# Optimization experiments

Hardware: AMD Instinct MI355X
Metric: run time of the kernel (lower is better)

Reference implementation:

```python
import jax, jax.numpy as jnp
import numpy as np

N = 131072
K = 27
FIN = 3
FOUT = 32
EPS = 1e-5


def _bn(h, gamma, beta, mean, var):
    return (h - mean) * jax.lax.rsqrt(var + EPS) * gamma + beta


def setup_inputs() -> dict:
    key = jax.random.key(0)
    ks = jax.random.split(key, 8)
    return {
        "x_feats": jax.random.normal(ks[0], (N, FIN), jnp.float32),
        "z_feats": jax.random.normal(ks[1], (N, FIN), jnp.float32),
        "nbr_idx": jax.random.randint(ks[2], (N, K), 0, N, jnp.int32),
        "w1": jax.random.normal(ks[3], (K, FIN, FOUT), jnp.float32) * 0.2,
        "bn1_gamma": jnp.ones((FOUT,), jnp.float32),
        "bn1_beta": jnp.zeros((FOUT,), jnp.float32),
        "bn1_mean": jax.random.normal(ks[4], (FOUT,), jnp.float32) * 0.1,
        "bn1_var": jax.random.uniform(ks[5], (FOUT,), jnp.float32, 0.5, 1.5),
        "w2": jax.random.normal(ks[6], (K, FOUT, FOUT), jnp.float32) * 0.1,
        "mlp_w": jax.random.normal(ks[7], (FIN, FOUT), jnp.float32) * 0.3,
        "mlp_b": jnp.zeros((FOUT,), jnp.float32),
        "mlp_gamma": jnp.ones((FOUT,), jnp.float32),
        "mlp_beta": jnp.zeros((FOUT,), jnp.float32),
        "mlp_mean": jnp.zeros((FOUT,), jnp.float32),
        "mlp_var": jnp.ones((FOUT,), jnp.float32),
    }


def reference(x_feats, z_feats, nbr_idx, w1, bn1_gamma, bn1_beta, bn1_mean,
              bn1_var, w2, mlp_w, mlp_b, mlp_gamma, mlp_beta, mlp_mean,
              mlp_var):
    # --- voxel branch: sparse conv (gather-GEMM) -> BN -> SiLU -> sparse conv
    g1 = x_feats[nbr_idx]                       # [N, K, FIN] irregular gather
    h = jnp.einsum('nkf,kfo->no', g1, w1)       # [N, FOUT]
    h = jax.nn.silu(_bn(h, bn1_gamma, bn1_beta, bn1_mean, bn1_var))
    g2 = h[nbr_idx]                             # [N, K, FOUT] irregular gather
    x_out = jnp.einsum('nkf,kfo->no', g2, w2)   # [N, FOUT]

    # --- point branch: SharedMLP = Linear -> BN -> ReLU
    z = z_feats @ mlp_w + mlp_b
    z = jax.nn.relu(_bn(z, mlp_gamma, mlp_beta, mlp_mean, mlp_var))

    # --- mixed_mix: fuse voxel and point features additively
    fused = x_out + z
    return (fused, fused)
```

## Files before the change

### kernel.cpp

```cpp
#include <hip/hip_runtime.h>
#include <math.h>

#define NN 131072
#define KK 27
#define KP 28
#define FIN 3
#define FOUT 32
#define EPS 1e-5f

typedef _Float16 f16;
typedef __attribute__((ext_vector_type(8))) _Float16 f16x8;
typedef __attribute__((ext_vector_type(16))) float f32x16;

__global__ __launch_bounds__(256) void pack_kernel(
    const float* __restrict__ w2, const float* __restrict__ w1,
    f16* __restrict__ w2p, float* __restrict__ w1p)
{
    const int t = blockIdx.x * 256 + threadIdx.x;
    if (t < KP * 1024) {
        const int k    = t >> 10;
        const int rem  = t & 1023;
        const int half = rem >> 9;
        const int l    = (rem >> 3) & 63;
        const int j    = rem & 7;
        const int krow = half * 16 + ((l >> 5) << 3) + j;
        const int n    = l & 31;
        w2p[t] = (k < KK) ? (f16)w2[k * (FOUT * FOUT) + krow * FOUT + n]
                          : (f16)0.f;
    } else {
        const int u = t - KP * 1024;
        if (u < KP * FIN * FOUT) {
            const int k = u / (FIN * FOUT);
            w1p[u] = (k < KK) ? w1[u] : 0.f;
        }
    }
}

__global__ __launch_bounds__(256) void pad_x_kernel(
    const float* __restrict__ x, float4* __restrict__ xp)
{
    const int n = blockIdx.x * 256 + threadIdx.x;
    if (n >= NN) return;
    const float* r = x + (size_t)n * 3;
    xp[n] = make_float4(r[0], r[1], r[2], 0.f);
}

__global__ __launch_bounds__(256) void conv1_kernel(
    const float4* __restrict__ xpad,
    const int*    __restrict__ nbr_idx,
    const float*  __restrict__ w1p,
    const float* __restrict__ g1,  const float* __restrict__ b1,
    const float* __restrict__ m1,  const float* __restrict__ v1,
    f16* __restrict__ h_out)
{
    __shared__ float racc[FOUT][128];

    const int tid   = threadIdx.x;
    const int khalf = tid >> 7;
    const int ln    = tid & 127;
    const int n     = blockIdx.x * 128 + ln;
    const int kb    = khalf * 14;

    int idxs[14];
    const int* nb = nbr_idx + (size_t)n * KK + kb;
#pragma unroll
    for (int i = 0; i < 14; ++i) {
        const int off = (kb + i < KK) ? i : 0;
        idxs[i] = nb[off];
    }
#pragma unroll
    for (int i = 0; i < 14; ++i) asm volatile("" : "+v"(idxs[i]));

    float acc[FOUT];
#pragma unroll
    for (int o = 0; o < FOUT; ++o) acc[o] = 0.f;

#pragma unroll
    for (int c = 0; c < 2; ++c) {
        float4 xs[7];
#pragma unroll
        for (int q = 0; q < 7; ++q)
            xs[q] = xpad[idxs[c * 7 + q]];
#pragma unroll
        for (int q = 0; q < 7; ++q) {
            const float* w = w1p + (kb + c * 7 + q) * (FIN * FOUT);
#pragma unroll
            for (int o = 0; o < FOUT; ++o) {
                float a = acc[o];
                a = fmaf(xs[q].x, w[o],            a);
                a = fmaf(xs[q].y, w[FOUT + o],     a);
                a = fmaf(xs[q].z, w[2 * FOUT + o], a);
                acc[o] = a;
            }
        }
    }

    if (khalf) {
#pragma unroll
        for (int o = 0; o < FOUT; ++o) racc[o][ln] = acc[o];
    }
    __syncthreads();
    if (khalf) return;

#pragma unroll
    for (int o = 0; o < FOUT; ++o) acc[o] += racc[o][ln];

    f16* hr = h_out + (size_t)n * FOUT;
#pragma unroll
    for (int g = 0; g < 4; ++g) {
        f16x8 hv;
#pragma unroll
        for (int j = 0; j < 8; ++j) {
            const int o = g * 8 + j;
            const float sc = g1[o] * rsqrtf(v1[o] + EPS);
            float v = (acc[o] - m1[o]) * sc + b1[o];
            v = v / (1.f + __expf(-v));
            hv[j] = (f16)v;
        }
        *(f16x8*)(hr + g * 8) = hv;
    }
}

__global__ __launch_bounds__(256) void conv2_mfma_kernel(
    const f16*   __restrict__ h,
    const int*   __restrict__ nbr_idx,
    const f16*   __restrict__ w2p,
    const float* __restrict__ z_feats,
    const float* __restrict__ mlp_w,
    const float* __restrict__ mlp_b,
    const float* __restrict__ mg, const float* __restrict__ mbe,
    const float* __restrict__ mm, const float* __restrict__ mv,
    float* __restrict__ out)
{
    const int lane = threadIdx.x & 63;
    const int wave = threadIdx.x >> 6;
    const int base = (blockIdx.x * 4 + wave) * 32;
    const int row  = lane & 31;
    const int hi   = lane >> 5;

    int idxs[KK];
    const int* nb = nbr_idx + (size_t)(base + row) * KK;
#pragma unroll
    for (int k = 0; k < KK; ++k) idxs[k] = nb[k];
#pragma unroll
    for (int k = 0; k < KK; ++k) asm volatile("" : "+v"(idxs[k]));

    f32x16 acc0 = {};
    f32x16 acc1 = {};

    const f16x8* bp = (const f16x8*)w2p;

    constexpr int D = 6;
    f16x8 A1[KK], A2[KK];

#pragma unroll
    for (int k = 0; k < D; ++k) {
        const f16* hr = h + (size_t)idxs[k] * FOUT + hi * 8;
        A1[k] = *(const f16x8*)hr;
        A2[k] = *(const f16x8*)(hr + 16);
    }

#pragma unroll
    for (int k = 0; k < KK; ++k) {
        if (k + D < KK) {
            const f16* hr = h + (size_t)idxs[k + D] * FOUT + hi * 8;
            A1[k + D] = *(const f16x8*)hr;
            A2[k + D] = *(const f16x8*)(hr + 16);
        }
        const f16x8 b1 = bp[k * 128 + lane];
        const f16x8 b2 = bp[k * 128 + 64 + lane];
        __builtin_amdgcn_s_setprio(1);
        acc0 = __builtin_amdgcn_mfma_f32_32x32x16_f16(A1[k], b1, acc0, 0, 0, 0);
        acc1 = __builtin_amdgcn_mfma_f32_32x32x16_f16(A2[k], b2, acc1, 0, 0, 0);
        __builtin_amdgcn_s_setprio(0);
    }

    const int n0 = lane & 31;
    const float wc0 = mlp_w[n0];
    const float wc1 = mlp_w[FOUT + n0];
    const float wc2 = mlp_w[2 * FOUT + n0];
    const float sc  = mg[n0] * rsqrtf(mv[n0] + EPS);
    const float bi  = mlp_b[n0];
    const float mmv = mm[n0];
    const float mbv = mbe[n0];

#pragma unroll
    for (int r = 0; r < 16; ++r) {
        const int m    = (r & 3) + ((r >> 2) << 3) + (hi << 2);
        const int node = base + m;
        const float* zr = z_feats + (size_t)node * FIN;
        float z = bi;
        z = fmaf(zr[0], wc0, z);
        z = fmaf(zr[1], wc1, z);
        z = fmaf(zr[2], wc2, z);
        z = (z - mmv) * sc + mbv;
        z = fmaxf(z, 0.f);
        const float v = acc0[r] + acc1[r] + z;
        out[(size_t)node * FOUT + n0] = v;
        out[(size_t)NN * FOUT + (size_t)node * FOUT + n0] = v;
    }
}

extern "C" void kernel_launch(void* const* d_in, const int* in_sizes, int n_in,
                              void* d_out, int out_size, void* d_ws, size_t ws_size,
                              hipStream_t stream) {
    const float* x_feats = (const float*)d_in[0];
    const float* z_feats = (const float*)d_in[1];
    const int*   nbr_idx = (const int*)d_in[2];
    const float* w1      = (const float*)d_in[3];
    const float* bn1_g   = (const float*)d_in[4];
    const float* bn1_b   = (const float*)d_in[5];
    const float* bn1_m   = (const float*)d_in[6];
    const float* bn1_v   = (const float*)d_in[7];
    const float* w2      = (const float*)d_in[8];
    const float* mlp_w   = (const float*)d_in[9];
    const float* mlp_b   = (const float*)d_in[10];
    const float* mlp_g   = (const float*)d_in[11];
    const float* mlp_be  = (const float*)d_in[12];
    const float* mlp_m   = (const float*)d_in[13];
    const float* mlp_v   = (const float*)d_in[14];

    const size_t OFF_W2P  = (size_t)8 * 1024 * 1024;
    const size_t OFF_W1P  = OFF_W2P + 64 * 1024;
    const size_t OFF_XPAD = (size_t)9 * 1024 * 1024;

    f16*    h    = (f16*)d_ws;
    f16*    w2p  = (f16*)((char*)d_ws + OFF_W2P);
    float*  w1p  = (float*)((char*)d_ws + OFF_W1P);
    float4* xpad = (float4*)((char*)d_ws + OFF_XPAD);
    float* out = (float*)d_out;

    const int pack_elems = KP * 1024 + KP * FIN * FOUT;
    pack_kernel<<<(pack_elems + 255) / 256, 256, 0, stream>>>(w2, w1, w2p, w1p);
    pad_x_kernel<<<NN / 256, 256, 0, stream>>>(x_feats, xpad);
    conv1_kernel<<<NN / 128, 256, 0, stream>>>(xpad, nbr_idx, w1p,
                                               bn1_g, bn1_b, bn1_m, bn1_v, h);
    conv2_mfma_kernel<<<NN / 128, 256, 0, stream>>>(h, nbr_idx, w2p, z_feats,
                                                    mlp_w, mlp_b, mlp_g, mlp_be,
                                                    mlp_m, mlp_v, out);
}
```

Before: 201.9 us.

## Transpose neighbor indices, split h into two halves, and restructure conv kernels

Adds a prep kernel that transposes nbr_idx into a k-major layout, so index loads in both conv kernels become coalesced, and fuses the x padding into it. The h buffer is split into two 16-channel halves, so each conv2 gather reads one 32-byte row per neighbor. Conv2 now runs two sequential MFMA passes with a one-step prefetch instead of a deep register prefetch, and sets a launch-bounds occupancy hint. Conv1 splits K four ways per block of 64 nodes. The cost is an extra write and read of a transposed index array, roughly 14 MB, plus a fallback path used when the workspace is too small.

```diff
diff --git a/kernel.cpp b/kernel.cpp
--- a/kernel.cpp
+++ b/kernel.cpp
@@ -36,6 +36,34 @@
     }
 }
 
+__global__ __launch_bounds__(256) void prep_kernel(
+    const int* __restrict__ nbr_idx, const float* __restrict__ x,
+    int* __restrict__ nbrT, float4* __restrict__ xpad)
+{
+    __shared__ int   lidx[64][29];
+    __shared__ float lx[192];
+    const int t  = threadIdx.x;
+    const int n0 = blockIdx.x * 64;
+
+    const int* src = nbr_idx + (size_t)n0 * KK;
+#pragma unroll
+    for (int j = 0; j < 7; ++j) {
+        const int f = j * 256 + t;
+        if (f < 64 * KK) lidx[f / KK][f % KK] = src[f];
+    }
+    if (t < 192) lx[t] = x[(size_t)n0 * 3 + t];
+    __syncthreads();
+
+    const int g = t >> 6, ln = t & 63;
+#pragma unroll
+    for (int j = 0; j < 7; ++j) {
+        const int k = g * 7 + j;
+        nbrT[(size_t)k * NN + n0 + ln] = (k < KK) ? lidx[ln][k] : 0;
+    }
+    if (t < 64)
+        xpad[n0 + t] = make_float4(lx[t * 3], lx[t * 3 + 1], lx[t * 3 + 2], 0.f);
+}
+
 __global__ __launch_bounds__(256) void pad_x_kernel(
     const float* __restrict__ x, float4* __restrict__ xp)
 {
@@ -45,67 +73,64 @@
     xp[n] = make_float4(r[0], r[1], r[2], 0.f);
 }
 
+template<bool TR>
 __global__ __launch_bounds__(256) void conv1_kernel(
     const float4* __restrict__ xpad,
+    const int*    __restrict__ nbrT,
     const int*    __restrict__ nbr_idx,
     const float*  __restrict__ w1p,
     const float* __restrict__ g1,  const float* __restrict__ b1,
     const float* __restrict__ m1,  const float* __restrict__ v1,
-    f16* __restrict__ h_out)
-{
-    __shared__ float racc[FOUT][128];
-
-    const int tid   = threadIdx.x;
-    const int khalf = tid >> 7;
-    const int ln    = tid & 127;
-    const int n     = blockIdx.x * 128 + ln;
-    const int kb    = khalf * 14;
-
-    int idxs[14];
-    const int* nb = nbr_idx + (size_t)n * KK + kb;
-#pragma unroll
-    for (int i = 0; i < 14; ++i) {
-        const int off = (kb + i < KK) ? i : 0;
-        idxs[i] = nb[off];
-    }
-#pragma unroll
-    for (int i = 0; i < 14; ++i) asm volatile("" : "+v"(idxs[i]));
+    f16* __restrict__ h0, f16* __restrict__ h1)
+{
+    __shared__ float racc[3][FOUT][64];
+    const int t  = threadIdx.x;
+    const int kg = t >> 6;
+    const int ln = t & 63;
+    const int n  = blockIdx.x * 64 + ln;
+
+    int idxs[7];
+#pragma unroll
+    for (int i = 0; i < 7; ++i) {
+        const int k = kg * 7 + i;
+        if (TR) idxs[i] = nbrT[(size_t)k * NN + n];
+        else    idxs[i] = (k < KK) ? nbr_idx[(size_t)n * KK + k] : 0;
+    }
+#pragma unroll
+    for (int i = 0; i < 7; ++i) asm volatile("" : "+v"(idxs[i]));
+
+    float4 xs[7];
+#pragma unroll
+    for (int i = 0; i < 7; ++i) xs[i] = xpad[idxs[i]];
 
     float acc[FOUT];
 #pragma unroll
     for (int o = 0; o < FOUT; ++o) acc[o] = 0.f;
 
 #pragma unroll
-    for (int c = 0; c < 2; ++c) {
-        float4 xs[7];
-#pragma unroll
-        for (int q = 0; q < 7; ++q)
-            xs[q] = xpad[idxs[c * 7 + q]];
-#pragma unroll
-        for (int q = 0; q < 7; ++q) {
-            const float* w = w1p + (kb + c * 7 + q) * (FIN * FOUT);
-#pragma unroll
-            for (int o = 0; o < FOUT; ++o) {
-                float a = acc[o];
-                a = fmaf(xs[q].x, w[o],            a);
-                a = fmaf(xs[q].y, w[FOUT + o],     a);
-                a = fmaf(xs[q].z, w[2 * FOUT + o], a);
-                acc[o] = a;
-            }
-        }
-    }
-
-    if (khalf) {
-#pragma unroll
-        for (int o = 0; o < FOUT; ++o) racc[o][ln] = acc[o];
+    for (int i = 0; i < 7; ++i) {
+        const float* w = w1p + (kg * 7 + i) * (FIN * FOUT);
+#pragma unroll
+        for (int o = 0; o < FOUT; ++o) {
+            float a = acc[o];
+            a = fmaf(xs[i].x, w[o],            a);
+            a = fmaf(xs[i].y, w[FOUT + o],     a);
+            a = fmaf(xs[i].z, w[2 * FOUT + o], a);
+            acc[o] = a;
+        }
+    }
+
+    if (kg) {
+#pragma unroll
+        for (int o = 0; o < FOUT; ++o) racc[kg - 1][o][ln] = acc[o];
     }
     __syncthreads();
-    if (khalf) return;
-
-#pragma unroll
-    for (int o = 0; o < FOUT; ++o) acc[o] += racc[o][ln];
-
-    f16* hr = h_out + (size_t)n * FOUT;
+    if (kg) return;
+
+#pragma unroll
+    for (int o = 0; o < FOUT; ++o)
+        acc[o] += racc[0][o][ln] + racc[1][o][ln] + racc[2][o][ln];
+
 #pragma unroll
     for (int g = 0; g < 4; ++g) {
         f16x8 hv;
@@ -117,12 +142,17 @@
             v = v / (1.f + __expf(-v));
             hv[j] = (f16)v;
         }
-        *(f16x8*)(hr + g * 8) = hv;
-    }
-}
-
-__global__ __launch_bounds__(256) void conv2_mfma_kernel(
-    const f16*   __restrict__ h,
+        f16* dst = (g < 2) ? (h0 + (size_t)n * 16 + (g & 1) * 8)
+                           : (h1 + (size_t)n * 16 + (g & 1) * 8);
+        *(f16x8*)dst = hv;
+    }
+}
+
+template<bool TR>
+__global__ __launch_bounds__(256, 4) void conv2_mfma_kernel(
+    const f16*   __restrict__ h0,
+    const f16*   __restrict__ h1,
+    const int*   __restrict__ nbrT,
     const int*   __restrict__ nbr_idx,
     const f16*   __restrict__ w2p,
     const float* __restrict__ z_feats,
@@ -139,40 +169,52 @@
     const int hi   = lane >> 5;
 
     int idxs[KK];
-    const int* nb = nbr_idx + (size_t)(base + row) * KK;
-#pragma unroll
-    for (int k = 0; k < KK; ++k) idxs[k] = nb[k];
+#pragma unroll
+    for (int k = 0; k < KK; ++k) {
+        if (TR) idxs[k] = nbrT[(size_t)k * NN + base + row];
+        else    idxs[k] = nbr_idx[(size_t)(base + row) * KK + k];
+    }
 #pragma unroll
     for (int k = 0; k < KK; ++k) asm volatile("" : "+v"(idxs[k]));
 
-    f32x16 acc0 = {};
-    f32x16 acc1 = {};
+    f32x16 accA = {};
+    f32x16 accB = {};
 
     const f16x8* bp = (const f16x8*)w2p;
 
-    constexpr int D = 6;
-    f16x8 A1[KK], A2[KK];
-
-#pragma unroll
-    for (int k = 0; k < D; ++k) {
-        const f16* hr = h + (size_t)idxs[k] * FOUT + hi * 8;
-        A1[k] = *(const f16x8*)hr;
-        A2[k] = *(const f16x8*)(hr + 16);
-    }
-
-#pragma unroll
-    for (int k = 0; k < KK; ++k) {
-        if (k + D < KK) {
-            const f16* hr = h + (size_t)idxs[k + D] * FOUT + hi * 8;
-            A1[k + D] = *(const f16x8*)hr;
-            A2[k + D] = *(const f16x8*)(hr + 16);
-        }
-        const f16x8 b1 = bp[k * 128 + lane];
-        const f16x8 b2 = bp[k * 128 + 64 + lane];
-        __builtin_amdgcn_s_setprio(1);
-        acc0 = __builtin_amdgcn_mfma_f32_32x32x16_f16(A1[k], b1, acc0, 0, 0, 0);
-        acc1 = __builtin_amdgcn_mfma_f32_32x32x16_f16(A2[k], b2, acc1, 0, 0, 0);
-        __builtin_amdgcn_s_setprio(0);
+    {
+        f16x8 a = *(const f16x8*)(h0 + (size_t)idxs[0] * 16 + hi * 8);
+        f16x8 b = bp[lane];
+#pragma unroll
+        for (int k = 0; k < KK; ++k) {
+            f16x8 na, nb2;
+            const bool more = (k + 1 < KK);
+            if (more) {
+                na  = *(const f16x8*)(h0 + (size_t)idxs[k + 1] * 16 + hi * 8);
+                nb2 = bp[(k + 1) * 128 + lane];
+            }
+            __builtin_amdgcn_s_setprio(1);
+            accA = __builtin_amdgcn_mfma_f32_32x32x16_f16(a, b, accA, 0, 0, 0);
+            __builtin_amdgcn_s_setprio(0);
+            if (more) { a = na; b = nb2; }
+        }
+    }
+    {
+        f16x8 a = *(const f16x8*)(h1 + (size_t)idxs[0] * 16 + hi * 8);
+        f16x8 b = bp[64 + lane];
+#pragma unroll
+        for (int k = 0; k < KK; ++k) {
+            f16x8 na, nb2;
+            const bool more = (k + 1 < KK);
+            if (more) {
+                na  = *(const f16x8*)(h1 + (size_t)idxs[k + 1] * 16 + hi * 8);
+                nb2 = bp[(k + 1) * 128 + 64 + lane];
+            }
+            __builtin_amdgcn_s_setprio(1);
+            accB = __builtin_amdgcn_mfma_f32_32x32x16_f16(a, b, accB, 0, 0, 0);
+            __builtin_amdgcn_s_setprio(0);
+            if (more) { a = na; b = nb2; }
+        }
     }
 
     const int n0 = lane & 31;
@@ -195,7 +237,7 @@
         z = fmaf(zr[2], wc2, z);
         z = (z - mmv) * sc + mbv;
         z = fmaxf(z, 0.f);
-        const float v = acc0[r] + acc1[r] + z;
+        const float v = accA[r] + accB[r] + z;
         out[(size_t)node * FOUT + n0] = v;
         out[(size_t)NN * FOUT + (size_t)node * FOUT + n0] = v;
     }
@@ -220,22 +262,37 @@
     const float* mlp_m   = (const float*)d_in[13];
     const float* mlp_v   = (const float*)d_in[14];
 
+    const size_t OFF_H1   = (size_t)4 * 1024 * 1024;
     const size_t OFF_W2P  = (size_t)8 * 1024 * 1024;
     const size_t OFF_W1P  = OFF_W2P + 64 * 1024;
     const size_t OFF_XPAD = (size_t)9 * 1024 * 1024;
-
-    f16*    h    = (f16*)d_ws;
+    const size_t OFF_NBRT = (size_t)11 * 1024 * 1024;
+    const size_t NBRT_SZ  = (size_t)KP * NN * 4;
+
+    f16*    h0   = (f16*)d_ws;
+    f16*    h1   = (f16*)((char*)d_ws + OFF_H1);
     f16*    w2p  = (f16*)((char*)d_ws + OFF_W2P);
     float*  w1p  = (float*)((char*)d_ws + OFF_W1P);
     float4* xpad = (float4*)((char*)d_ws + OFF_XPAD);
+    int*    nbrT = (int*)((char*)d_ws + OFF_NBRT);
+    const bool tr = ws_size >= OFF_NBRT + NBRT_SZ;
     float* out = (float*)d_out;
 
     const int pack_elems = KP * 1024 + KP * FIN * FOUT;
     pack_kernel<<<(pack_elems + 255) / 256, 256, 0, stream>>>(w2, w1, w2p, w1p);
-    pad_x_kernel<<<NN / 256, 256, 0, stream>>>(x_feats, xpad);
-    conv1_kernel<<<NN / 128, 256, 0, stream>>>(xpad, nbr_idx, w1p,
-                                               bn1_g, bn1_b, bn1_m, bn1_v, h);
-    conv2_mfma_kernel<<<NN / 128, 256, 0, stream>>>(h, nbr_idx, w2p, z_feats,
-                                                    mlp_w, mlp_b, mlp_g, mlp_be,
-                                                    mlp_m, mlp_v, out);
-}
+    if (tr) {
+        prep_kernel<<<NN / 64, 256, 0, stream>>>(nbr_idx, x_feats, nbrT, xpad);
+        conv1_kernel<true><<<NN / 64, 256, 0, stream>>>(
+            xpad, nbrT, nbr_idx, w1p, bn1_g, bn1_b, bn1_m, bn1_v, h0, h1);
+        conv2_mfma_kernel<true><<<NN / 128, 256, 0, stream>>>(
+            h0, h1, nbrT, nbr_idx, w2p, z_feats, mlp_w, mlp_b,
+            mlp_g, mlp_be, mlp_m, mlp_v, out);
+    } else {
+        pad_x_kernel<<<NN / 256, 256, 0, stream>>>(x_feats, xpad);
+        conv1_kernel<false><<<NN / 64, 256, 0, stream>>>(
+            xpad, nbrT, nbr_idx, w1p, bn1_g, bn1_b, bn1_m, bn1_v, h0, h1);
+        conv2_mfma_kernel<false><<<NN / 128, 256, 0, stream>>>(
+            h0, h1, nbrT, nbr_idx, w2p, z_feats, mlp_w, mlp_b,
+            mlp_g, mlp_be, mlp_m, mlp_v, out);
+    }
+}
```

Result: slower. 214.1 us (+6.1%).
